# Performance work log

Hardware: AMD Instinct MI355X
Metric: run time of the kernel (lower is better)

Reference implementation:

```python
import jax, jax.numpy as jnp
import numpy as np

B, N, DIN, DH = 16, 1024, 128, 256
SENTINEL = 10**8  # stands in for torch's float('inf') init; never matches any bin


def setup_inputs() -> dict:
    key = jax.random.key(0)
    ks = jax.random.split(key, 8)
    features = jax.random.normal(ks[0], (B, N, DIN), jnp.float32)
    mask = jnp.ones((B, N), dtype=bool)
    dm = jax.random.randint(ks[1], (B, N, N), 0, 10)
    # map one bin value to the 'unreachable' sentinel 9999 used by the module
    dm = jnp.where(dm == 9, 9999, dm).astype(jnp.int32)
    tst_token = (jax.random.normal(ks[2], (1, 1, DIN), jnp.float32) * 0.02)
    codebook = jax.random.normal(ks[3], (6, DIN), jnp.float32)
    W1 = jax.random.normal(ks[4], (DIN, DH), jnp.float32) / np.sqrt(DIN).astype(np.float32)
    b1 = jnp.zeros((DH,), jnp.float32)
    W2 = jax.random.normal(ks[5], (DH, 1), jnp.float32) / np.sqrt(DH).astype(np.float32)
    b2 = jnp.zeros((1,), jnp.float32)
    return {
        "features": features, "mask": mask, "distance_matrix": dm,
        "tst_token": tst_token, "codebook": codebook,
        "W1": W1, "b1": b1, "W2": W2, "b2": b2,
    }


def reference(features, mask, distance_matrix, tst_token, codebook, W1, b1, W2, b2):
    b, n, d = features.shape
    # prepend test token: (B, N+1, DIN)
    input_X = jnp.concatenate([jnp.broadcast_to(tst_token, (b, 1, d)), features], axis=1)
    # build augmented distance matrix input_D of shape (B, N+1, N+1)
    row0 = distance_matrix[:, 0, :]                      # (B, N)
    upd = jnp.where(row0 == 9999, 9999, row0 + 1)        # tst-token distances
    D = jnp.full((b, n + 1, n + 1), SENTINEL, jnp.int32)
    D = D.at[:, 0, 1:].set(upd)
    D = D.at[:, 1:, 0].set(upd)
    D = D.at[:, 1:, 1:].set(distance_matrix)
    D = D.at[:, 0, 0].set(0)
    input_MASK = jnp.concatenate([jnp.ones((b, 1), dtype=bool), mask], axis=1)
    # bias_mlp output is constant per codebook row -> compute the 6 scalars once
    scalars = (jax.nn.relu(codebook @ W1 + b1) @ W2 + b2)[:, 0]        # (6,)
    lut = jnp.concatenate([scalars, jnp.zeros((1,), scalars.dtype)])   # index 6 -> 0 (unbinned)
    # bins: dist in 0..4 -> lut[dist]; dist == 9999 -> lut[5]; else -> 0
    sel = jnp.where(D == 9999, 5, jnp.where(D < 5, D, 6))
    bias_mat = lut[sel]                                               # (B, N+1, N+1)
    return input_X, input_MASK, bias_mat
```

## Files before the change

kernel.cpp:

```cpp
#include <hip/hip_runtime.h>
#include <hip/hip_bf16.h>

#define NB     16
#define NN     1024
#define NP1    1025
#define DIN    128
#define DH     256

#define OFF1   2099200
#define OFF2   2115600

#define ROWS_PER_BLK 4
#define NB_BIAS  (NB * NP1 / ROWS_PER_BLK)
#define NB_COPY  (NB * 16)
#define NB_MASK  NB

__global__ __launch_bounds__(256) void lut_kernel(
    const float* __restrict__ cb,
    const float* __restrict__ W1,
    const float* __restrict__ b1,
    const float* __restrict__ W2,
    const float* __restrict__ b2,
    float* __restrict__ lut)
{
    const int c = blockIdx.x;
    const int t = threadIdx.x;
    const float* __restrict__ cbr = cb + c * DIN;
    float acc = 0.f;
    #pragma unroll
    for (int k = 0; k < DIN; k += 8) {
        float a0 = W1[(k + 0) * DH + t];
        float a1 = W1[(k + 1) * DH + t];
        float a2 = W1[(k + 2) * DH + t];
        float a3 = W1[(k + 3) * DH + t];
        float a4 = W1[(k + 4) * DH + t];
        float a5 = W1[(k + 5) * DH + t];
        float a6 = W1[(k + 6) * DH + t];
        float a7 = W1[(k + 7) * DH + t];
        acc = fmaf(cbr[k + 0], a0, acc);
        acc = fmaf(cbr[k + 1], a1, acc);
        acc = fmaf(cbr[k + 2], a2, acc);
        acc = fmaf(cbr[k + 3], a3, acc);
        acc = fmaf(cbr[k + 4], a4, acc);
        acc = fmaf(cbr[k + 5], a5, acc);
        acc = fmaf(cbr[k + 6], a6, acc);
        acc = fmaf(cbr[k + 7], a7, acc);
    }
    float h = fmaxf(acc + b1[t], 0.f);
    float p = h * W2[t];
    #pragma unroll
    for (int off = 32; off; off >>= 1)
        p += __shfl_down(p, off);
    __shared__ float part[4];
    if ((t & 63) == 0) part[t >> 6] = p;
    __syncthreads();
    if (t == 0) {
        lut[c] = part[0] + part[1] + part[2] + part[3] + b2[0];
        if (c == 0) lut[6] = 0.f;
    }
}

__global__ __launch_bounds__(256) void main_kernel(
    const float* __restrict__ feat,
    const int* __restrict__ mask,
    const int* __restrict__ dm,
    const float* __restrict__ tst,
    const float* __restrict__ lut,
    float* __restrict__ out)
{
    const int bid = blockIdx.x;
    const int tid = threadIdx.x;

    if (bid < NB_BIAS) {
        __shared__ float sl[7];
        if (tid < 7) sl[tid] = lut[tid];
        __syncthreads();

        const int g0 = bid * ROWS_PER_BLK;
        #pragma unroll
        for (int k = 0; k < ROWS_PER_BLK; ++k) {
            const int g = g0 + k;
            const int b = g / NP1;
            const int i = g - b * NP1;
            float* __restrict__ orow = out + OFF2 + (size_t)g * NP1;
            const int* __restrict__ dmb = dm + (size_t)b * (NN * NN);

            if (i == 0) {
                if (tid == 0) orow[0] = sl[0];
                int r0 = dmb[tid];
                int r1 = dmb[tid + 256];
                int r2 = dmb[tid + 512];
                int r3 = dmb[tid + 768];
                orow[1 + tid]       = (r0 == 9999) ? sl[5] : (r0 <= 3 ? sl[r0 + 1] : sl[6]);
                orow[1 + tid + 256] = (r1 == 9999) ? sl[5] : (r1 <= 3 ? sl[r1 + 1] : sl[6]);
                orow[1 + tid + 512] = (r2 == 9999) ? sl[5] : (r2 <= 3 ? sl[r2 + 1] : sl[6]);
                orow[1 + tid + 768] = (r3 == 9999) ? sl[5] : (r3 <= 3 ? sl[r3 + 1] : sl[6]);
            } else {
                if (tid == 0) {
                    int r = dmb[i - 1];
                    orow[0] = (r == 9999) ? sl[5] : (r <= 3 ? sl[r + 1] : sl[6]);
                }
                const int* __restrict__ dr = dmb + (size_t)(i - 1) * NN;
                int d0 = dr[tid];
                int d1 = dr[tid + 256];
                int d2 = dr[tid + 512];
                int d3 = dr[tid + 768];
                orow[1 + tid]       = (d0 == 9999) ? sl[5] : (d0 < 5 ? sl[d0] : sl[6]);
                orow[1 + tid + 256] = (d1 == 9999) ? sl[5] : (d1 < 5 ? sl[d1] : sl[6]);
                orow[1 + tid + 512] = (d2 == 9999) ? sl[5] : (d2 < 5 ? sl[d2] : sl[6]);
                orow[1 + tid + 768] = (d3 == 9999) ? sl[5] : (d3 < 5 ? sl[d3] : sl[6]);
            }
        }
    } else if (bid < NB_BIAS + NB_COPY) {
        const int cid  = bid - NB_BIAS;
        const int b    = cid >> 4;
        const int chnk = cid & 15;
        const float4* __restrict__ src =
            (const float4*)(feat + (size_t)b * (NN * DIN)) + (size_t)chnk * 2048;
        float4* __restrict__ dst =
            (float4*)(out + (size_t)b * (NP1 * DIN) + DIN) + (size_t)chnk * 2048;
        #pragma unroll
        for (int u = 0; u < 8; ++u)
            dst[tid + 256 * u] = src[tid + 256 * u];
        if (chnk == 0 && tid < 32) {
            ((float4*)(out + (size_t)b * (NP1 * DIN)))[tid] =
                ((const float4*)tst)[tid];
        }
    } else {
        const int b = bid - (NB_BIAS + NB_COPY);
        float* __restrict__ om = out + OFF1 + b * NP1;
        const int* __restrict__ mb = mask + (size_t)b * NN;
        if (tid == 0) om[0] = 1.0f;
        for (int j = tid; j < NN; j += 256)
            om[1 + j] = mb[j] ? 1.0f : 0.0f;
    }
}

extern "C" void kernel_launch(void* const* d_in, const int* in_sizes, int n_in,
                              void* d_out, int out_size, void* d_ws, size_t ws_size,
                              hipStream_t stream) {
    const float* feat = (const float*)d_in[0];
    const int*   mask = (const int*)d_in[1];
    const int*   dm   = (const int*)d_in[2];
    const float* tst  = (const float*)d_in[3];
    const float* cb   = (const float*)d_in[4];
    const float* W1   = (const float*)d_in[5];
    const float* b1   = (const float*)d_in[6];
    const float* W2   = (const float*)d_in[7];
    const float* b2   = (const float*)d_in[8];
    float* out = (float*)d_out;
    float* lut = (float*)d_ws;

    lut_kernel<<<6, 256, 0, stream>>>(cb, W1, b1, W2, b2, lut);
    main_kernel<<<NB_BIAS + NB_COPY + NB_MASK, 256, 0, stream>>>(
        feat, mask, dm, tst, lut, out);
}
```

Measured before the change: 34.33 us.

## Move feature copy and mask into LUT kernel; split bias into own kernel

The feature copy and mask conversion move out of the main kernel and into the first launch, next to the LUT computation. All six LUT rows are now computed in a single block that loads W1 once. The bias-matrix pass becomes a separate kernel with 8 rows per block instead of 4. The goal is to hide the copy work behind the tiny LUT launch and shorten the second kernel, at the cost of a serial single-block LUT computation on the first kernel's critical path.

```diff
diff --git a/kernel.cpp b/kernel.cpp
--- a/kernel.cpp
+++ b/kernel.cpp
@@ -10,109 +10,61 @@
 #define OFF1   2099200
 #define OFF2   2115600
 
-#define ROWS_PER_BLK 4
-#define NB_BIAS  (NB * NP1 / ROWS_PER_BLK)
-#define NB_COPY  (NB * 16)
-#define NB_MASK  NB
+#define A_COPY0  1
+#define A_MASK0  (A_COPY0 + 256)
+#define A_GRID   (A_MASK0 + NB)
 
-__global__ __launch_bounds__(256) void lut_kernel(
+#define RPB      8
+#define B_GRID   (NB * NP1 / RPB)
+
+__global__ __launch_bounds__(256) void pre_kernel(
+    const float* __restrict__ feat,
+    const int* __restrict__ mask,
+    const float* __restrict__ tst,
     const float* __restrict__ cb,
     const float* __restrict__ W1,
     const float* __restrict__ b1,
     const float* __restrict__ W2,
     const float* __restrict__ b2,
+    float* __restrict__ out,
     float* __restrict__ lut)
-{
-    const int c = blockIdx.x;
-    const int t = threadIdx.x;
-    const float* __restrict__ cbr = cb + c * DIN;
-    float acc = 0.f;
-    #pragma unroll
-    for (int k = 0; k < DIN; k += 8) {
-        float a0 = W1[(k + 0) * DH + t];
-        float a1 = W1[(k + 1) * DH + t];
-        float a2 = W1[(k + 2) * DH + t];
-        float a3 = W1[(k + 3) * DH + t];
-        float a4 = W1[(k + 4) * DH + t];
-        float a5 = W1[(k + 5) * DH + t];
-        float a6 = W1[(k + 6) * DH + t];
-        float a7 = W1[(k + 7) * DH + t];
-        acc = fmaf(cbr[k + 0], a0, acc);
-        acc = fmaf(cbr[k + 1], a1, acc);
-        acc = fmaf(cbr[k + 2], a2, acc);
-        acc = fmaf(cbr[k + 3], a3, acc);
-        acc = fmaf(cbr[k + 4], a4, acc);
-        acc = fmaf(cbr[k + 5], a5, acc);
-        acc = fmaf(cbr[k + 6], a6, acc);
-        acc = fmaf(cbr[k + 7], a7, acc);
-    }
-    float h = fmaxf(acc + b1[t], 0.f);
-    float p = h * W2[t];
-    #pragma unroll
-    for (int off = 32; off; off >>= 1)
-        p += __shfl_down(p, off);
-    __shared__ float part[4];
-    if ((t & 63) == 0) part[t >> 6] = p;
-    __syncthreads();
-    if (t == 0) {
-        lut[c] = part[0] + part[1] + part[2] + part[3] + b2[0];
-        if (c == 0) lut[6] = 0.f;
-    }
-}
-
-__global__ __launch_bounds__(256) void main_kernel(
-    const float* __restrict__ feat,
-    const int* __restrict__ mask,
-    const int* __restrict__ dm,
-    const float* __restrict__ tst,
-    const float* __restrict__ lut,
-    float* __restrict__ out)
 {
     const int bid = blockIdx.x;
     const int tid = threadIdx.x;
 
-    if (bid < NB_BIAS) {
-        __shared__ float sl[7];
-        if (tid < 7) sl[tid] = lut[tid];
+    if (bid == 0) {
+        const int t = tid;
+        float acc0 = 0.f, acc1 = 0.f, acc2 = 0.f, acc3 = 0.f, acc4 = 0.f, acc5 = 0.f;
+        #pragma unroll 4
+        for (int k = 0; k < DIN; ++k) {
+            float w = W1[(size_t)k * DH + t];
+            acc0 = fmaf(cb[0 * DIN + k], w, acc0);
+            acc1 = fmaf(cb[1 * DIN + k], w, acc1);
+            acc2 = fmaf(cb[2 * DIN + k], w, acc2);
+            acc3 = fmaf(cb[3 * DIN + k], w, acc3);
+            acc4 = fmaf(cb[4 * DIN + k], w, acc4);
+            acc5 = fmaf(cb[5 * DIN + k], w, acc5);
+        }
+        const float bb = b1[t], w2 = W2[t];
+        float h[6] = {
+            fmaxf(acc0 + bb, 0.f) * w2, fmaxf(acc1 + bb, 0.f) * w2,
+            fmaxf(acc2 + bb, 0.f) * w2, fmaxf(acc3 + bb, 0.f) * w2,
+            fmaxf(acc4 + bb, 0.f) * w2, fmaxf(acc5 + bb, 0.f) * w2 };
+        __shared__ float red[6][4];
+        #pragma unroll
+        for (int c = 0; c < 6; ++c) {
+            float p = h[c];
+            #pragma unroll
+            for (int off = 32; off; off >>= 1)
+                p += __shfl_down(p, off);
+            if ((tid & 63) == 0) red[c][tid >> 6] = p;
+        }
         __syncthreads();
-
-        const int g0 = bid * ROWS_PER_BLK;
-        #pragma unroll
-        for (int k = 0; k < ROWS_PER_BLK; ++k) {
-            const int g = g0 + k;
-            const int b = g / NP1;
-            const int i = g - b * NP1;
-            float* __restrict__ orow = out + OFF2 + (size_t)g * NP1;
-            const int* __restrict__ dmb = dm + (size_t)b * (NN * NN);
-
-            if (i == 0) {
-                if (tid == 0) orow[0] = sl[0];
-                int r0 = dmb[tid];
-                int r1 = dmb[tid + 256];
-                int r2 = dmb[tid + 512];
-                int r3 = dmb[tid + 768];
-                orow[1 + tid]       = (r0 == 9999) ? sl[5] : (r0 <= 3 ? sl[r0 + 1] : sl[6]);
-                orow[1 + tid + 256] = (r1 == 9999) ? sl[5] : (r1 <= 3 ? sl[r1 + 1] : sl[6]);
-                orow[1 + tid + 512] = (r2 == 9999) ? sl[5] : (r2 <= 3 ? sl[r2 + 1] : sl[6]);
-                orow[1 + tid + 768] = (r3 == 9999) ? sl[5] : (r3 <= 3 ? sl[r3 + 1] : sl[6]);
-            } else {
-                if (tid == 0) {
-                    int r = dmb[i - 1];
-                    orow[0] = (r == 9999) ? sl[5] : (r <= 3 ? sl[r + 1] : sl[6]);
-                }
-                const int* __restrict__ dr = dmb + (size_t)(i - 1) * NN;
-                int d0 = dr[tid];
-                int d1 = dr[tid + 256];
-                int d2 = dr[tid + 512];
-                int d3 = dr[tid + 768];
-                orow[1 + tid]       = (d0 == 9999) ? sl[5] : (d0 < 5 ? sl[d0] : sl[6]);
-                orow[1 + tid + 256] = (d1 == 9999) ? sl[5] : (d1 < 5 ? sl[d1] : sl[6]);
-                orow[1 + tid + 512] = (d2 == 9999) ? sl[5] : (d2 < 5 ? sl[d2] : sl[6]);
-                orow[1 + tid + 768] = (d3 == 9999) ? sl[5] : (d3 < 5 ? sl[d3] : sl[6]);
-            }
-        }
-    } else if (bid < NB_BIAS + NB_COPY) {
-        const int cid  = bid - NB_BIAS;
+        if (tid < 6)
+            lut[tid] = red[tid][0] + red[tid][1] + red[tid][2] + red[tid][3] + b2[0];
+        if (tid == 6) lut[6] = 0.f;
+    } else if (bid < A_MASK0) {
+        const int cid  = bid - A_COPY0;
         const int b    = cid >> 4;
         const int chnk = cid & 15;
         const float4* __restrict__ src =
@@ -127,12 +79,59 @@
                 ((const float4*)tst)[tid];
         }
     } else {
-        const int b = bid - (NB_BIAS + NB_COPY);
+        const int b = bid - A_MASK0;
         float* __restrict__ om = out + OFF1 + b * NP1;
         const int* __restrict__ mb = mask + (size_t)b * NN;
         if (tid == 0) om[0] = 1.0f;
         for (int j = tid; j < NN; j += 256)
             om[1 + j] = mb[j] ? 1.0f : 0.0f;
+    }
+}
+
+__global__ __launch_bounds__(256) void bias_kernel(
+    const int* __restrict__ dm,
+    const float* __restrict__ lut,
+    float* __restrict__ out)
+{
+    const int tid = threadIdx.x;
+    __shared__ float sl[7];
+    if (tid < 7) sl[tid] = lut[tid];
+    __syncthreads();
+
+    const int g0 = blockIdx.x * RPB;
+    #pragma unroll
+    for (int k = 0; k < RPB; ++k) {
+        const int g = g0 + k;
+        const int b = g / NP1;
+        const int i = g - b * NP1;
+        float* __restrict__ orow = out + OFF2 + (size_t)g * NP1;
+        const int* __restrict__ dmb = dm + (size_t)b * (NN * NN);
+
+        if (i == 0) {
+            if (tid == 0) orow[0] = sl[0];
+            int r0 = dmb[tid];
+            int r1 = dmb[tid + 256];
+            int r2 = dmb[tid + 512];
+            int r3 = dmb[tid + 768];
+            orow[1 + tid]       = (r0 == 9999) ? sl[5] : (r0 <= 3 ? sl[r0 + 1] : sl[6]);
+            orow[1 + tid + 256] = (r1 == 9999) ? sl[5] : (r1 <= 3 ? sl[r1 + 1] : sl[6]);
+            orow[1 + tid + 512] = (r2 == 9999) ? sl[5] : (r2 <= 3 ? sl[r2 + 1] : sl[6]);
+            orow[1 + tid + 768] = (r3 == 9999) ? sl[5] : (r3 <= 3 ? sl[r3 + 1] : sl[6]);
+        } else {
+            if (tid == 0) {
+                int r = dmb[i - 1];
+                orow[0] = (r == 9999) ? sl[5] : (r <= 3 ? sl[r + 1] : sl[6]);
+            }
+            const int* __restrict__ dr = dmb + (size_t)(i - 1) * NN;
+            int d0 = dr[tid];
+            int d1 = dr[tid + 256];
+            int d2 = dr[tid + 512];
+            int d3 = dr[tid + 768];
+            orow[1 + tid]       = (d0 == 9999) ? sl[5] : (d0 < 5 ? sl[d0] : sl[6]);
+            orow[1 + tid + 256] = (d1 == 9999) ? sl[5] : (d1 < 5 ? sl[d1] : sl[6]);
+            orow[1 + tid + 512] = (d2 == 9999) ? sl[5] : (d2 < 5 ? sl[d2] : sl[6]);
+            orow[1 + tid + 768] = (d3 == 9999) ? sl[5] : (d3 < 5 ? sl[d3] : sl[6]);
+        }
     }
 }
 
@@ -151,7 +150,7 @@
     float* out = (float*)d_out;
     float* lut = (float*)d_ws;
 
-    lut_kernel<<<6, 256, 0, stream>>>(cb, W1, b1, W2, b2, lut);
-    main_kernel<<<NB_BIAS + NB_COPY + NB_MASK, 256, 0, stream>>>(
-        feat, mask, dm, tst, lut, out);
+    pre_kernel<<<A_GRID, 256, 0, stream>>>(feat, mask, tst, cb, W1, b1, W2, b2,
+                                           out, lut);
+    bias_kernel<<<B_GRID, 256, 0, stream>>>(dm, lut, out);
 }
```

After: 43.06 us. +25.4%, slower.
